# Optimization experiments

Hardware: AMD Instinct MI355X
Metric: run time of the kernel (lower is better)

Reference implementation:

```python
import jax, jax.numpy as jnp
import numpy as np

NUM_T = 1000      # diffusion timesteps
TIME_DIM = 16     # gaussian time embedding size
DIST_DIM = 16     # gaussian distance embedding size


def _gsmear(x, stop, num_g):
    # GaussianSmearing with linearly spaced centers in [0, stop]
    offsets = jnp.linspace(0.0, stop, num_g)
    coeff = -0.5 / (offsets[1] - offsets[0]) ** 2
    return jnp.exp(coeff * (x[:, None] - offsets[None, :]) ** 2)


def setup_inputs():
    key = jax.random.key(0)
    ks = jax.random.split(key, 20)
    N, EH, G = 20000, 100000, 1000          # nodes, halfedges, graphs
    NT, ND, ED, L, NE = 16, 256, 128, 2, 5   # node types, node_dim, edge_dim, blocks, edge types
    h_node = jax.nn.one_hot(jax.random.randint(ks[0], (N,), 0, NT), NT, dtype=jnp.float32)
    pos_node = jax.random.normal(ks[1], (N, 3), dtype=jnp.float32) * 3.0
    batch_node = jnp.sort(jax.random.randint(ks[2], (N,), 0, G))
    half = jax.random.randint(ks[3], (2, EH), 0, N)
    edge_index = jnp.concatenate([half, half[::-1]], axis=1)  # halfedges + flipped
    bh = jnp.sort(jax.random.randint(ks[4], (EH,), 0, G))
    batch_edge = jnp.concatenate([bh, bh], axis=0)
    t = jax.random.randint(ks[5], (G,), 0, NUM_T)

    def w(k, shape):
        fan_in = shape[-2] if len(shape) > 1 else shape[-1]
        return jax.random.normal(k, shape, dtype=jnp.float32) / np.sqrt(fan_in)

    e_in = ED + 2 * ND + DIST_DIM + 1
    return {
        'h_node': h_node, 'pos_node': pos_node, 'batch_node': batch_node,
        'edge_index': edge_index, 'batch_edge': batch_edge, 't': t,
        'W_node_emb': w(ks[6], (NT, ND - TIME_DIM)),
        'W_edge_emb': w(ks[7], (2 * NT, ED - TIME_DIM)),
        'We1': w(ks[8], (L, e_in, ED)), 'be1': jnp.zeros((L, ED), jnp.float32),
        'We2': w(ks[9], (L, ED, ED)), 'be2': jnp.zeros((L, ED), jnp.float32),
        'Wm': w(ks[10], (L, ND + ED, ND)), 'bm': jnp.zeros((L, ND), jnp.float32),
        'Wn1': w(ks[11], (L, 2 * ND + 1, ND)), 'bn1': jnp.zeros((L, ND), jnp.float32),
        'Wn2': w(ks[12], (L, ND, ND)), 'bn2': jnp.zeros((L, ND), jnp.float32),
        'Wd1': w(ks[13], (ED + ND, ED)), 'bd1': jnp.zeros((ED,), jnp.float32),
        'Wd2': w(ks[14], (ED, ED)), 'bd2': jnp.zeros((ED,), jnp.float32),
        'Wd3': w(ks[15], (ED, NE)), 'bd3': jnp.zeros((NE,), jnp.float32),
    }


def reference(h_node, pos_node, batch_node, edge_index, batch_edge, t,
              W_node_emb, W_edge_emb, We1, be1, We2, be2, Wm, bm,
              Wn1, bn1, Wn2, bn2, Wd1, bd1, Wd2, bd2, Wd3, bd3):
    src, dst = edge_index[0], edge_index[1]
    N = h_node.shape[0]
    L = We1.shape[0]

    # edge input features: concat of endpoint node features (gather)
    h_e0 = jnp.concatenate([h_node[src], h_node[dst]], axis=-1)

    tn = t[batch_node].astype(jnp.float32)  # per-node timestep
    te = t[batch_edge].astype(jnp.float32)  # per-edge timestep
    # linear embed + gaussian-smeared time embedding
    h_n = jnp.concatenate([h_node @ W_node_emb, _gsmear(tn, float(NUM_T), TIME_DIM)], axis=-1)
    h_e = jnp.concatenate([h_e0 @ W_edge_emb, _gsmear(te, float(NUM_T), TIME_DIM)], axis=-1)
    node_time = (tn / NUM_T)[:, None]
    edge_time = (te / NUM_T)[:, None]

    # geometric edge features
    d = jnp.linalg.norm(pos_node[dst] - pos_node[src], axis=-1)
    dist_emb = _gsmear(d, 10.0, DIST_DIM)

    # NodeEdgeNet: alternating edge / node residual updates
    for l in range(L):
        e_in = jnp.concatenate([h_e, h_n[src], h_n[dst], dist_emb, edge_time], axis=-1)
        h_e = h_e + jax.nn.relu(e_in @ We1[l] + be1[l]) @ We2[l] + be2[l]
        msg = jax.nn.relu(jnp.concatenate([h_n[src], h_e], axis=-1) @ Wm[l] + bm[l])
        agg = jax.ops.segment_sum(msg, dst, num_segments=N)
        n_in = jnp.concatenate([h_n, agg, node_time], axis=-1)
        h_n = h_n + jax.nn.relu(n_in @ Wn1[l] + bn1[l]) @ Wn2[l] + bn2[l]

    # symmetrize halfedges and decode edge types
    nh = h_e.shape[0] // 2
    h_ext = jnp.concatenate([h_e[:nh] + h_e[nh:],
                             h_n[src[:nh]] + h_n[dst[:nh]]], axis=-1)
    h = jax.nn.relu(h_ext @ Wd1 + bd1)
    h = jax.nn.relu(h @ Wd2 + bd2)
    return h @ Wd3 + bd3
```

## Files before the change

### kernel.cpp

```cpp
#include <hip/hip_runtime.h>
#include <math.h>


typedef __attribute__((ext_vector_type(8)))  short bf16x8;
typedef __attribute__((ext_vector_type(16))) float f32x16;

__device__ __forceinline__ float b2f(unsigned short u) {
    union { float f; unsigned int i; } x; x.i = ((unsigned int)u) << 16; return x.f;
}
__device__ __forceinline__ unsigned short f2b(float f) {
    union { float f; unsigned int i; } x; x.f = f;
    unsigned int r = x.i + 0x7fffu + ((x.i >> 16) & 1u);
    return (unsigned short)(r >> 16);
}
__device__ __forceinline__ bf16x8 ld8(const unsigned short* p) { return *(const bf16x8*)p; }
__device__ __forceinline__ bf16x8 zero8() { bf16x8 r = {0,0,0,0,0,0,0,0}; return r; }
__device__ __forceinline__ bf16x8 add8(bf16x8 a, bf16x8 b) {
    bf16x8 r;
#pragma unroll
    for (int j = 0; j < 8; j++) r[j] = (short)f2b(b2f((unsigned short)a[j]) + b2f((unsigned short)b[j]));
    return r;
}

#define MFMA4(ACC, A0, A1, B0, B1)                                                   \
    ACC[0][0] = __builtin_amdgcn_mfma_f32_32x32x16_bf16(A0, B0, ACC[0][0], 0, 0, 0); \
    ACC[0][1] = __builtin_amdgcn_mfma_f32_32x32x16_bf16(A0, B1, ACC[0][1], 0, 0, 0); \
    ACC[1][0] = __builtin_amdgcn_mfma_f32_32x32x16_bf16(A1, B0, ACC[1][0], 0, 0, 0); \
    ACC[1][1] = __builtin_amdgcn_mfma_f32_32x32x16_bf16(A1, B1, ACC[1][1], 0, 0, 0);

#define LANE_SETUP()                                  \
    const int tid  = threadIdx.x;                     \
    const int lane = tid & 63;                        \
    const int wave = tid >> 6;                        \
    const int wm = wave >> 1, wn = wave & 1;          \
    const int l31 = lane & 31, l5 = lane >> 5;        \
    (void)wm; (void)wn; (void)lane;

#define PIPELINE4(NITER, FETCH, ACC)                                  \
    {                                                                 \
        bf16x8 pa0[2], pb0[2], pa1[2], pb1[2], pa2[2], pb2[2];        \
        FETCH(0, pa0, pb0);                                           \
        if (1 < (NITER)) FETCH(1, pa1, pb1);                          \
        _Pragma("unroll")                                             \
        for (int i = 0; i < (NITER); i++) {                           \
            if (i + 2 < (NITER)) FETCH(i + 2, pa2, pb2);              \
            MFMA4(ACC, pa0[0], pa0[1], pb0[0], pb0[1]);               \
            pa0[0] = pa1[0]; pa0[1] = pa1[1];                         \
            pb0[0] = pb1[0]; pb0[1] = pb1[1];                         \
            pa1[0] = pa2[0]; pa1[1] = pa2[1];                         \
            pb1[0] = pb2[0]; pb1[1] = pb2[1];                         \
        }                                                             \
    }

#define PIPELINE2(NITER, FETCH, ACC)                                  \
    {                                                                 \
        bf16x8 pa0, pb0[2], pa1, pb1[2], pa2, pb2[2];                 \
        FETCH(0, pa0, pb0);                                           \
        if (1 < (NITER)) FETCH(1, pa1, pb1);                          \
        _Pragma("unroll")                                             \
        for (int i = 0; i < (NITER); i++) {                           \
            if (i + 2 < (NITER)) FETCH(i + 2, pa2, pb2);              \
            ACC[0] = __builtin_amdgcn_mfma_f32_32x32x16_bf16(pa0, pb0[0], ACC[0], 0, 0, 0); \
            ACC[1] = __builtin_amdgcn_mfma_f32_32x32x16_bf16(pa0, pb0[1], ACC[1], 0, 0, 0); \
            pa0 = pa1; pb0[0] = pb1[0]; pb0[1] = pb1[1];              \
            pa1 = pa2; pb1[0] = pb2[0]; pb1[1] = pb2[1];              \
        }                                                             \
    }

__global__ void zero_i32_k(int* p, int n) {
    int i = blockIdx.x * 256 + threadIdx.x;
    if (i < n) p[i] = 0;
}
__global__ void hist_k(const int* __restrict__ dst, int* __restrict__ cnt, int E) {
    int e = blockIdx.x * 256 + threadIdx.x;
    if (e < E) atomicAdd(&cnt[dst[e]], 1);
}
__global__ __launch_bounds__(256) void scan_k(int* __restrict__ cnt, int N) {
    __shared__ int s[256];
    const int tidx  = threadIdx.x;
    const int chunk = (N + 255) / 256;
    const int lo = tidx * chunk;
    const int hi = (lo + chunk < N) ? lo + chunk : N;
    int sum = 0;
    for (int i = lo; i < hi; i++) sum += cnt[i];
    s[tidx] = sum;
    __syncthreads();
    for (int d = 1; d < 256; d <<= 1) {
        int t = (tidx >= d) ? s[tidx - d] : 0;
        __syncthreads();
        s[tidx] += t;
        __syncthreads();
    }
    int base = s[tidx] - sum;
    for (int i = lo; i < hi; i++) {
        int c = cnt[i];
        cnt[i] = base;
        base += c;
    }
}
__global__ void fill_k(const int* __restrict__ src, const int* __restrict__ dst,
                       const int* __restrict__ batch_edge, int* __restrict__ cur,
                       int* __restrict__ eids, int* __restrict__ pos,
                       int* __restrict__ srcp, int* __restrict__ dstp,
                       int* __restrict__ bep, int E) {
    int e = blockIdx.x * 256 + threadIdx.x;
    if (e < E) {
        int p = atomicAdd(&cur[dst[e]], 1);
        eids[p] = e;
        pos[e]  = p;
        srcp[p] = src[e];
        dstp[p] = dst[e];
        bep[p]  = batch_edge[e];
    }
}
__global__ void pad_k(int* eids, int* srcp, int* dstp, int* bep, int E, int Epad) {
    int i = E + blockIdx.x * 256 + threadIdx.x;
    if (i < Epad) { eids[i] = -1; srcp[i] = 0; dstp[i] = -1; bep[i] = 0; }
}

__global__ void typ_k(const float* __restrict__ h_node, int* __restrict__ typ, int N) {
    int i = blockIdx.x * 256 + threadIdx.x;
    if (i >= N) return;
    int ty = 0;
#pragma unroll
    for (int k = 0; k < 16; k++) if (h_node[i * 16 + k] > 0.5f) ty = k;
    typ[i] = ty;
}

struct TrDesc { const float* W; unsigned short* Wt; int K, N, Kpad; };
struct TrAll  { TrDesc d[12]; };

__global__ __launch_bounds__(256) void tr_all_k(TrAll a) {
    TrDesc t = a.d[blockIdx.y];
    int total = t.N * t.Kpad;
    for (int i = blockIdx.x * 256 + threadIdx.x; i < total; i += gridDim.x * 256) {
        int n = i / t.Kpad, k = i - n * t.Kpad;
        float v = (k < t.K) ? t.W[(size_t)k * t.N + n] : 0.f;
        t.Wt[(size_t)n * t.Kpad + k] = f2b(v);
    }
}

__global__ void embed_node_k(const int* __restrict__ typ,
                             const float* __restrict__ Wn,
                             const int* __restrict__ batch_node,
                             const int* __restrict__ t,
                             unsigned short* __restrict__ h_n, int N) {
    int idx = blockIdx.x * 256 + threadIdx.x;
    if (idx >= N * 32) return;
    int row = idx >> 5, seg = idx & 31;
    bf16x8 v;
    if (seg < 30) {
        const float* w = Wn + (size_t)typ[row] * 240 + seg * 8;
#pragma unroll
        for (int j = 0; j < 8; j++) v[j] = (short)f2b(w[j]);
    } else {
        float x = (float)t[batch_node[row]];
#pragma unroll
        for (int j = 0; j < 8; j++) {
            int col = seg * 8 + j;
            float dx = x - (1000.0f / 15.0f) * (float)(col - 240);
            v[j] = (short)f2b(expf(-1.125e-4f * dx * dx));
        }
    }
    *(bf16x8*)&h_n[(size_t)row * 256 + seg * 8] = v;
}

__global__ void embed_edge_k(const int* __restrict__ typ,
                             const float* __restrict__ We,
                             const int* __restrict__ srcp,
                             const int* __restrict__ dstp,
                             const int* __restrict__ bep,
                             const int* __restrict__ t,
                             unsigned short* __restrict__ h_e, int E) {
    int idx = blockIdx.x * 256 + threadIdx.x;
    if (idx >= E * 16) return;
    int row = idx >> 4, seg = idx & 15;
    bf16x8 v;
    if (seg < 14) {
        int d0 = dstp[row]; if (d0 < 0) d0 = 0;
        const float* ws = We + (size_t)typ[srcp[row]] * 112 + seg * 8;
        const float* wd = We + (size_t)(16 + typ[d0]) * 112 + seg * 8;
#pragma unroll
        for (int j = 0; j < 8; j++) v[j] = (short)f2b(ws[j] + wd[j]);
    } else {
        float x = (float)t[bep[row]];
#pragma unroll
        for (int j = 0; j < 8; j++) {
            int col = seg * 8 + j;
            float dx = x - (1000.0f / 15.0f) * (float)(col - 112);
            v[j] = (short)f2b(expf(-1.125e-4f * dx * dx));
        }
    }
    *(bf16x8*)&h_e[(size_t)row * 128 + seg * 8] = v;
}

__global__ __launch_bounds__(256) void edge_fused_k(
    unsigned short* __restrict__ h_e, const unsigned short* __restrict__ h_n,
    const unsigned short* __restrict__ Wt1, const float* __restrict__ be1,
    const unsigned short* __restrict__ Wt2, const float* __restrict__ be2,
    const float* __restrict__ pos, const int* __restrict__ srcp,
    const int* __restrict__ dstp, const int* __restrict__ t,
    const int* __restrict__ bep, int E)
{
    __shared__ __align__(16) unsigned short H[128][136];
    LANE_SETUP();
    const int row0 = blockIdx.x * 128;

    int   rr[2]; const unsigned short *hep[2], *hns[2], *hnd[2];
    float dist[2], timev[2]; bool ok[2];
    rr[0] = row0 + wm * 64 + l31; rr[1] = rr[0] + 32;
#pragma unroll
    for (int h = 0; h < 2; h++) {
        ok[h] = rr[h] < E;
        int r = ok[h] ? rr[h] : 0;
        int s = srcp[r], d = dstp[r] < 0 ? 0 : dstp[r];
        hep[h] = h_e + (size_t)r * 128;
        hns[h] = h_n + (size_t)s * 256;
        hnd[h] = h_n + (size_t)d * 256;
        float dx = pos[d * 3 + 0] - pos[s * 3 + 0];
        float dy = pos[d * 3 + 1] - pos[s * 3 + 1];
        float dz = pos[d * 3 + 2] - pos[s * 3 + 2];
        dist[h]  = sqrtf(dx * dx + dy * dy + dz * dz);
        timev[h] = (float)t[bep[r]] * 1e-3f;
    }

    const unsigned short* W1a = Wt1 + (size_t)(wn * 64 + l31) * 672;
    const unsigned short* W1b = Wt1 + (size_t)(wn * 64 + 32 + l31) * 672;

    f32x16 acc[2][2] = {};
#define EF_FETCH(i, A, B)                                                      \
    {                                                                          \
        const int c = 2 * (i) + l5;                                            \
        _Pragma("unroll")                                                      \
        for (int h = 0; h < 2; h++) {                                          \
            if (!ok[h])      A[h] = zero8();                                   \
            else if (c < 16) A[h] = ld8(hep[h] + (c << 3));                    \
            else if (c < 48) A[h] = ld8(hns[h] + ((c - 16) << 3));             \
            else if (c < 80) A[h] = ld8(hnd[h] + ((c - 48) << 3));             \
            else if (c < 82) {                                                 \
                bf16x8 rv;                                                     \
                _Pragma("unroll")                                              \
                for (int j = 0; j < 8; j++) {                                  \
                    float u = dist[h] - (10.0f / 15.0f) * (float)((c - 80) * 8 + j); \
                    rv[j] = (short)f2b(expf(-1.125f * u * u));                 \
                }                                                              \
                A[h] = rv;                                                     \
            } else if (c == 82) { A[h] = zero8(); A[h][0] = (short)f2b(timev[h]); } \
            else A[h] = zero8();                                               \
        }                                                                      \
        B[0] = ld8(W1a + (c << 3));                                            \
        B[1] = ld8(W1b + (c << 3));                                            \
    }
    PIPELINE4(42, EF_FETCH, acc)
#undef EF_FETCH

#pragma unroll
    for (int mt = 0; mt < 2; mt++)
#pragma unroll
        for (int nt = 0; nt < 2; nt++)
#pragma unroll
            for (int r = 0; r < 16; r++) {
                int lrow = wm * 64 + mt * 32 + (r & 3) + 8 * (r >> 2) + 4 * l5;
                int col  = wn * 64 + nt * 32 + l31;
                float v = acc[mt][nt][r] + be1[col];
                H[lrow][col] = f2b(fmaxf(v, 0.f));
            }
    __syncthreads();

    const unsigned short* W2a = Wt2 + (size_t)(wn * 64 + l31) * 128;
    const unsigned short* W2b = Wt2 + (size_t)(wn * 64 + 32 + l31) * 128;
    f32x16 acc2[2][2] = {};
#define EF2_FETCH(i, A, B)                                          \
    {                                                               \
        const int c = 2 * (i) + l5;                                 \
        A[0] = *(const bf16x8*)&H[wm * 64 + l31][c << 3];           \
        A[1] = *(const bf16x8*)&H[wm * 64 + 32 + l31][c << 3];      \
        B[0] = ld8(W2a + (c << 3));                                 \
        B[1] = ld8(W2b + (c << 3));                                 \
    }
    PIPELINE4(8, EF2_FETCH, acc2)
#undef EF2_FETCH

#pragma unroll
    for (int mt = 0; mt < 2; mt++)
#pragma unroll
        for (int nt = 0; nt < 2; nt++)
#pragma unroll
            for (int r = 0; r < 16; r++) {
                int lrow = wm * 64 + mt * 32 + (r & 3) + 8 * (r >> 2) + 4 * l5;
                int grow = row0 + lrow;
                if (grow >= E) continue;
                int col = wn * 64 + nt * 32 + l31;
                size_t off = (size_t)grow * 128 + col;
                float v = acc2[mt][nt][r] + be2[col] + b2f(h_e[off]);
                h_e[off] = f2b(v);
            }
}

__global__ __launch_bounds__(256) void msg_k(
    const unsigned short* __restrict__ h_e, const unsigned short* __restrict__ h_n,
    const unsigned short* __restrict__ Wtm, const float* __restrict__ bm,
    const int* __restrict__ srcp, const int* __restrict__ dstp,
    float* __restrict__ agg, int E, int nRowTiles)
{
    __shared__ __align__(16) char smem[33024 + 512];
    unsigned short (*As)[8][8] = (unsigned short(*)[8][8])smem;
    unsigned short (*Bs)[8][8] = (unsigned short(*)[8][8])(smem + 16384);
    float (*T)[129] = (float(*)[129])smem;
    int* dstv = (int*)(smem + 33024);

    LANE_SETUP();
    const int b    = blockIdx.x;
    const int rowt = (b >> 4) * 8 + (b & 7);
    const int colh = (b >> 3) & 1;
    if (rowt >= nRowTiles) return;
    const int row0 = rowt * 128;
    const int col0 = colh * 128;

    if (tid < 128) dstv[tid] = dstp[row0 + tid];

    const int srow = tid >> 3, sks = tid & 7;

    f32x16 acc[2][2] = {};
    for (int kc = 0; kc < 6; kc++) {
        const int cg = kc * 8 + sks;
#pragma unroll
        for (int p = 0; p < 4; p++) {
            int row = srow + p * 32;
            int r   = row0 + row;
            bf16x8 v;
            if (r < E) {
                if (cg < 32) v = ld8(h_n + (size_t)srcp[r] * 256 + (cg << 3));
                else         v = ld8(h_e + (size_t)r * 128 + ((cg - 32) << 3));
            } else v = zero8();
            *(bf16x8*)&As[row][sks ^ (row & 7)][0] = v;
        }
#pragma unroll
        for (int p = 0; p < 4; p++) {
            int col = srow + p * 32;
            bf16x8 v = ld8(Wtm + (size_t)(col0 + col) * 384 + (cg << 3));
            *(bf16x8*)&Bs[col][sks ^ (col & 7)][0] = v;
        }
        __syncthreads();
#pragma unroll
        for (int s = 0; s < 4; s++) {
            const int ks  = s * 2 + l5;
            const int ra0 = wm * 64 + l31, ra1 = ra0 + 32;
            const int ca0 = wn * 64 + l31, ca1 = ca0 + 32;
            bf16x8 a0 = *(const bf16x8*)&As[ra0][ks ^ (ra0 & 7)][0];
            bf16x8 a1 = *(const bf16x8*)&As[ra1][ks ^ (ra1 & 7)][0];
            bf16x8 b0 = *(const bf16x8*)&Bs[ca0][ks ^ (ca0 & 7)][0];
            bf16x8 b1 = *(const bf16x8*)&Bs[ca1][ks ^ (ca1 & 7)][0];
            MFMA4(acc, a0, a1, b0, b1);
        }
        __syncthreads();
    }

    for (int ph = 0; ph < 2; ph++) {
        __syncthreads();
        if (wm == ph) {
#pragma unroll
            for (int mt = 0; mt < 2; mt++)
#pragma unroll
                for (int nt = 0; nt < 2; nt++)
#pragma unroll
                    for (int r = 0; r < 16; r++) {
                        int lrow = mt * 32 + (r & 3) + 8 * (r >> 2) + 4 * l5;
                        int col  = wn * 64 + nt * 32 + l31;
                        T[lrow][col] = acc[mt][nt][r] + bm[col0 + col];
                    }
        }
        __syncthreads();
        const int col = tid & 127, seg = tid >> 7;
        const int gcol = col0 + col;
        float run = 0.f; int prev = -1;
#pragma unroll 4
        for (int i = 0; i < 32; i++) {
            int lr = seg * 32 + i;
            int d  = dstv[ph * 64 + lr];
            float v = fmaxf(T[lr][col], 0.f);
            if (d != prev) {
                if (prev >= 0 && run != 0.f) atomicAdd(&agg[(size_t)prev * 256 + gcol], run);
                run = 0.f; prev = d;
            }
            if (d >= 0) run += v;
        }
        if (prev >= 0 && run != 0.f) atomicAdd(&agg[(size_t)prev * 256 + gcol], run);
    }
}

__global__ __launch_bounds__(256) void nin_k(
    const unsigned short* __restrict__ h_n, const float* __restrict__ agg,
    const unsigned short* __restrict__ Wtn1, const float* __restrict__ bn1,
    const int* __restrict__ batch_node, const int* __restrict__ t,
    unsigned short* __restrict__ Hn, int N)
{
    LANE_SETUP();
    const int row0 = blockIdx.x * 64;
    const int col0 = blockIdx.y * 128;

    int rr = row0 + wm * 32 + l31;
    bool ok = rr < N;
    int r = ok ? rr : 0;
    float timev = (float)t[batch_node[r]] * 1e-3f;
    const unsigned short* hp = h_n + (size_t)r * 256;
    const float*          ap = agg + (size_t)r * 256;

    const unsigned short* Wa = Wtn1 + (size_t)(col0 + wn * 64 + l31) * 544;
    const unsigned short* Wb = Wtn1 + (size_t)(col0 + wn * 64 + 32 + l31) * 544;

    f32x16 acc[2] = {};
#define NIN_FETCH(i, A, B)                                              \
    {                                                                   \
        const int c = 2 * (i) + l5;                                     \
        if (!ok) A = zero8();                                           \
        else if (c < 32) A = ld8(hp + (c << 3));                        \
        else if (c < 64) {                                              \
            const float* q = ap + ((c - 32) << 3);                      \
            bf16x8 v;                                                   \
            _Pragma("unroll")                                           \
            for (int j = 0; j < 8; j++) v[j] = (short)f2b(q[j]);        \
            A = v;                                                      \
        } else if (c == 64) { A = zero8(); A[0] = (short)f2b(timev); }  \
        else A = zero8();                                               \
        B[0] = ld8(Wa + (c << 3));                                      \
        B[1] = ld8(Wb + (c << 3));                                      \
    }
    PIPELINE2(34, NIN_FETCH, acc)
#undef NIN_FETCH

#pragma unroll
    for (int nt = 0; nt < 2; nt++)
#pragma unroll
        for (int r2 = 0; r2 < 16; r2++) {
            int lrow = wm * 32 + (r2 & 3) + 8 * (r2 >> 2) + 4 * l5;
            int grow = row0 + lrow;
            if (grow >= N) continue;
            int col = col0 + wn * 64 + nt * 32 + l31;
            float v = fmaxf(acc[nt][r2] + bn1[col], 0.f);
            Hn[(size_t)grow * 256 + col] = f2b(v);
        }
}

__global__ __launch_bounds__(256) void node_plain_k(
    const unsigned short* __restrict__ Hn, const unsigned short* __restrict__ Wtn2,
    const float* __restrict__ bn2, unsigned short* __restrict__ h_n, int N)
{
    LANE_SETUP();
    const int row0 = blockIdx.x * 64;
    const int col0 = blockIdx.y * 128;

    int rr = row0 + wm * 32 + l31;
    bool ok = rr < N;
    const unsigned short* hp = Hn + (size_t)(ok ? rr : 0) * 256;

    const unsigned short* Wa = Wtn2 + (size_t)(col0 + wn * 64 + l31) * 256;
    const unsigned short* Wb = Wtn2 + (size_t)(col0 + wn * 64 + 32 + l31) * 256;

    f32x16 acc[2] = {};
#define NP_FETCH(i, A, B)                          \
    {                                              \
        const int c = 2 * (i) + l5;                \
        A = ok ? ld8(hp + (c << 3)) : zero8();     \
        B[0] = ld8(Wa + (c << 3));                 \
        B[1] = ld8(Wb + (c << 3));                 \
    }
    PIPELINE2(16, NP_FETCH, acc)
#undef NP_FETCH

#pragma unroll
    for (int nt = 0; nt < 2; nt++)
#pragma unroll
        for (int r2 = 0; r2 < 16; r2++) {
            int lrow = wm * 32 + (r2 & 3) + 8 * (r2 >> 2) + 4 * l5;
            int grow = row0 + lrow;
            if (grow >= N) continue;
            int col = col0 + wn * 64 + nt * 32 + l31;
            size_t off = (size_t)grow * 256 + col;
            float v = acc[nt][r2] + bn2[col] + b2f(h_n[off]);
            h_n[off] = f2b(v);
        }
}

__global__ __launch_bounds__(256) void dec_fused_k(
    const unsigned short* __restrict__ h_e, const unsigned short* __restrict__ h_n,
    const unsigned short* __restrict__ Wtd1, const float* __restrict__ bd1,
    const unsigned short* __restrict__ Wtd2, const float* __restrict__ bd2,
    const float* __restrict__ Wd3, const float* __restrict__ bd3,
    const int* __restrict__ src, const int* __restrict__ dst,
    const int* __restrict__ pos, float* __restrict__ out, int nh)
{
    __shared__ __align__(16) unsigned short H1[128][136];
    __shared__ __align__(16) unsigned short H2[128][136];
    LANE_SETUP();
    const int row0 = blockIdx.x * 128;

    int rr[2]; const unsigned short *he1[2], *he2[2], *hns[2], *hnd[2]; bool ok[2];
    rr[0] = row0 + wm * 64 + l31; rr[1] = rr[0] + 32;
#pragma unroll
    for (int h = 0; h < 2; h++) {
        ok[h] = rr[h] < nh;
        int r = ok[h] ? rr[h] : 0;
        he1[h] = h_e + (size_t)pos[r] * 128;
        he2[h] = h_e + (size_t)pos[r + nh] * 128;
        hns[h] = h_n + (size_t)src[r] * 256;
        hnd[h] = h_n + (size_t)dst[r] * 256;
    }

    const unsigned short* W1a = Wtd1 + (size_t)(wn * 64 + l31) * 384;
    const unsigned short* W1b = Wtd1 + (size_t)(wn * 64 + 32 + l31) * 384;

    f32x16 acc[2][2] = {};
#define DC_FETCH(i, A, B)                                                            \
    {                                                                                \
        const int c = 2 * (i) + l5;                                                  \
        _Pragma("unroll")                                                            \
        for (int h = 0; h < 2; h++) {                                                \
            if (!ok[h])      A[h] = zero8();                                         \
            else if (c < 16) A[h] = add8(ld8(he1[h] + (c << 3)), ld8(he2[h] + (c << 3))); \
            else             A[h] = add8(ld8(hns[h] + ((c - 16) << 3)), ld8(hnd[h] + ((c - 16) << 3))); \
        }                                                                            \
        B[0] = ld8(W1a + (c << 3));                                                  \
        B[1] = ld8(W1b + (c << 3));                                                  \
    }
    PIPELINE4(24, DC_FETCH, acc)
#undef DC_FETCH

#pragma unroll
    for (int mt = 0; mt < 2; mt++)
#pragma unroll
        for (int nt = 0; nt < 2; nt++)
#pragma unroll
            for (int r = 0; r < 16; r++) {
                int lrow = wm * 64 + mt * 32 + (r & 3) + 8 * (r >> 2) + 4 * l5;
                int col  = wn * 64 + nt * 32 + l31;
                H1[lrow][col] = f2b(fmaxf(acc[mt][nt][r] + bd1[col], 0.f));
            }
    __syncthreads();

    const unsigned short* W2a = Wtd2 + (size_t)(wn * 64 + l31) * 128;
    const unsigned short* W2b = Wtd2 + (size_t)(wn * 64 + 32 + l31) * 128;
    f32x16 acc2[2][2] = {};
#define DC2_FETCH(i, A, B)                                          \
    {                                                               \
        const int c = 2 * (i) + l5;                                 \
        A[0] = *(const bf16x8*)&H1[wm * 64 + l31][c << 3];          \
        A[1] = *(const bf16x8*)&H1[wm * 64 + 32 + l31][c << 3];     \
        B[0] = ld8(W2a + (c << 3));                                 \
        B[1] = ld8(W2b + (c << 3));                                 \
    }
    PIPELINE4(8, DC2_FETCH, acc2)
#undef DC2_FETCH

#pragma unroll
    for (int mt = 0; mt < 2; mt++)
#pragma unroll
        for (int nt = 0; nt < 2; nt++)
#pragma unroll
            for (int r = 0; r < 16; r++) {
                int lrow = wm * 64 + mt * 32 + (r & 3) + 8 * (r >> 2) + 4 * l5;
                int col  = wn * 64 + nt * 32 + l31;
                H2[lrow][col] = f2b(fmaxf(acc2[mt][nt][r] + bd2[col], 0.f));
            }
    __syncthreads();

    if (tid < 128) {
        int grow = row0 + tid;
        if (grow < nh) {
            float a5[5] = {0.f, 0.f, 0.f, 0.f, 0.f};
            for (int ks = 0; ks < 16; ks++) {
                bf16x8 hv = *(const bf16x8*)&H2[tid][ks << 3];
#pragma unroll
                for (int j = 0; j < 8; j++) {
                    float a = b2f((unsigned short)hv[j]);
                    int   k = ks * 8 + j;
#pragma unroll
                    for (int c5 = 0; c5 < 5; c5++) a5[c5] += a * Wd3[k * 5 + c5];
                }
            }
#pragma unroll
            for (int c5 = 0; c5 < 5; c5++) out[(size_t)grow * 5 + c5] = a5[c5] + bd3[c5];
        }
    }
}


__global__ void zero_k(float* p, long n) {
    long i = (long)blockIdx.x * 256 + threadIdx.x;
    if (i < n) p[i] = 0.f;
}


extern "C" void kernel_launch(void* const* d_in, const int* in_sizes, int n_in,
                              void* d_out, int out_size, void* d_ws, size_t ws_size,
                              hipStream_t stream) {
    const float* h_node     = (const float*)d_in[0];
    const float* pos_node   = (const float*)d_in[1];
    const int*   batch_node = (const int*)d_in[2];
    const int*   edge_index = (const int*)d_in[3];
    const int*   batch_edge = (const int*)d_in[4];
    const int*   t          = (const int*)d_in[5];
    const float* W_node_emb = (const float*)d_in[6];
    const float* W_edge_emb = (const float*)d_in[7];
    const float* We1 = (const float*)d_in[8];
    const float* be1 = (const float*)d_in[9];
    const float* We2 = (const float*)d_in[10];
    const float* be2 = (const float*)d_in[11];
    const float* Wm  = (const float*)d_in[12];
    const float* bm  = (const float*)d_in[13];
    const float* Wn1 = (const float*)d_in[14];
    const float* bn1 = (const float*)d_in[15];
    const float* Wn2 = (const float*)d_in[16];
    const float* bn2 = (const float*)d_in[17];
    const float* Wd1 = (const float*)d_in[18];
    const float* bd1 = (const float*)d_in[19];
    const float* Wd2 = (const float*)d_in[20];
    const float* bd2 = (const float*)d_in[21];
    const float* Wd3 = (const float*)d_in[22];
    const float* bd3 = (const float*)d_in[23];

    const int N  = in_sizes[0] / 16;
    const int E  = in_sizes[3] / 2;
    const int nh = E / 2;
    const int* src = edge_index;
    const int* dst = edge_index + E;

    const int gE   = (E + 127) / 128;
    const int gE8  = ((gE + 7) / 8) * 8;
    const int gN64 = (N + 63) / 64;
    const int Epad = gE * 128;

    float* agg  = (float*)d_ws;
    int*   cnt  = (int*)(agg + (size_t)N * 256);
    int*   eids = cnt + N;
    int*   pos  = eids + Epad;
    int*   srcp = pos + Epad;
    int*   dstp = srcp + Epad;
    int*   bep  = dstp + Epad;
    int*   typ  = bep + Epad;
    unsigned short* h_e = (unsigned short*)(typ + N);
    unsigned short* h_n = h_e + (size_t)E * 128;
    unsigned short* Hn  = h_n + (size_t)N * 256;
    unsigned short* Wt1  = Hn + (size_t)N * 256;
    unsigned short* Wt2  = Wt1 + 2 * 128 * 672;
    unsigned short* Wtm  = Wt2 + 2 * 128 * 128;
    unsigned short* Wtn1 = Wtm + 2 * 256 * 384;
    unsigned short* Wtn2 = Wtn1 + 2 * 256 * 544;
    unsigned short* Wtd1 = Wtn2 + 2 * 256 * 256;
    unsigned short* Wtd2 = Wtd1 + 128 * 384;

    zero_i32_k<<<(N + 255) / 256, 256, 0, stream>>>(cnt, N);
    hist_k<<<(E + 255) / 256, 256, 0, stream>>>(dst, cnt, E);
    scan_k<<<1, 256, 0, stream>>>(cnt, N);
    fill_k<<<(E + 255) / 256, 256, 0, stream>>>(src, dst, batch_edge, cnt,
                                                eids, pos, srcp, dstp, bep, E);
    if (Epad > E) pad_k<<<1, 256, 0, stream>>>(eids, srcp, dstp, bep, E, Epad);
    typ_k<<<(N + 255) / 256, 256, 0, stream>>>(h_node, typ, N);

    TrAll ta;
    for (int l = 0; l < 2; l++) {
        ta.d[l * 5 + 0] = { We1 + (size_t)l * 657 * 128, Wt1 + (size_t)l * 128 * 672, 657, 128, 672 };
        ta.d[l * 5 + 1] = { We2 + (size_t)l * 128 * 128, Wt2 + (size_t)l * 128 * 128, 128, 128, 128 };
        ta.d[l * 5 + 2] = { Wm  + (size_t)l * 384 * 256, Wtm + (size_t)l * 256 * 384, 384, 256, 384 };
        ta.d[l * 5 + 3] = { Wn1 + (size_t)l * 513 * 256, Wtn1 + (size_t)l * 256 * 544, 513, 256, 544 };
        ta.d[l * 5 + 4] = { Wn2 + (size_t)l * 256 * 256, Wtn2 + (size_t)l * 256 * 256, 256, 256, 256 };
    }
    ta.d[10] = { Wd1, Wtd1, 384, 128, 384 };
    ta.d[11] = { Wd2, Wtd2, 128, 128, 128 };
    tr_all_k<<<dim3(48, 12), 256, 0, stream>>>(ta);

    embed_node_k<<<(N * 32 + 255) / 256, 256, 0, stream>>>(typ, W_node_emb, batch_node, t, h_n, N);
    embed_edge_k<<<(E * 16 + 255) / 256, 256, 0, stream>>>(typ, W_edge_emb, srcp, dstp, bep, t, h_e, E);

    for (int l = 0; l < 2; l++) {
        edge_fused_k<<<gE, 256, 0, stream>>>(
            h_e, h_n, Wt1 + (size_t)l * 128 * 672, be1 + l * 128,
            Wt2 + (size_t)l * 128 * 128, be2 + l * 128,
            pos_node, srcp, dstp, t, bep, E);

        zero_k<<<(int)(((long)N * 256 + 255) / 256), 256, 0, stream>>>(agg, (long)N * 256);
        msg_k<<<gE8 * 2, 256, 0, stream>>>(
            h_e, h_n, Wtm + (size_t)l * 256 * 384, bm + l * 256, srcp, dstp, agg, E, gE);

        nin_k<<<dim3(gN64, 2), 256, 0, stream>>>(
            h_n, agg, Wtn1 + (size_t)l * 256 * 544, bn1 + l * 256, batch_node, t, Hn, N);

        node_plain_k<<<dim3(gN64, 2), 256, 0, stream>>>(
            Hn, Wtn2 + (size_t)l * 256 * 256, bn2 + l * 256, h_n, N);
    }

    dec_fused_k<<<(nh + 127) / 128, 256, 0, stream>>>(
        h_e, h_n, Wtd1, bd1, Wtd2, bd2, Wd3, bd3, src, dst, pos, (float*)d_out, nh);
}
```

Measured before the change: 1.027 ms.

## Stage gathered edge and decoder inputs through swizzled shared memory tiles

The first GEMM of the edge and decoder kernels now stages both the gathered A rows and the weight B tiles into XOR-swizzled shared memory in K-chunks of 64, rather than each wave loading A and B fragments straight from global memory. Each row and weight element is fetched once per block instead of once per wave that uses it, which removes the duplicate gather traffic across the wave grid. In exchange the kernels add two barriers per K-chunk and lose the register-prefetch pipeline, so load latency is no longer overlapped with MFMA work. The distance embedding is now recomputed per chunk inside the loader.

```diff
diff --git a/kernel.cpp b/kernel.cpp
--- a/kernel.cpp
+++ b/kernel.cpp
@@ -202,57 +202,76 @@
     const int* __restrict__ dstp, const int* __restrict__ t,
     const int* __restrict__ bep, int E)
 {
-    __shared__ __align__(16) unsigned short H[128][136];
+    __shared__ __align__(16) char smem[128 * 136 * 2];
+    unsigned short (*As)[8][8] = (unsigned short(*)[8][8])smem;
+    unsigned short (*Bs)[8][8] = (unsigned short(*)[8][8])(smem + 16384);
+    unsigned short (*H)[136]   = (unsigned short(*)[136])smem;
+
     LANE_SETUP();
     const int row0 = blockIdx.x * 128;
-
-    int   rr[2]; const unsigned short *hep[2], *hns[2], *hnd[2];
-    float dist[2], timev[2]; bool ok[2];
-    rr[0] = row0 + wm * 64 + l31; rr[1] = rr[0] + 32;
-#pragma unroll
-    for (int h = 0; h < 2; h++) {
-        ok[h] = rr[h] < E;
-        int r = ok[h] ? rr[h] : 0;
-        int s = srcp[r], d = dstp[r] < 0 ? 0 : dstp[r];
-        hep[h] = h_e + (size_t)r * 128;
-        hns[h] = h_n + (size_t)s * 256;
-        hnd[h] = h_n + (size_t)d * 256;
-        float dx = pos[d * 3 + 0] - pos[s * 3 + 0];
-        float dy = pos[d * 3 + 1] - pos[s * 3 + 1];
-        float dz = pos[d * 3 + 2] - pos[s * 3 + 2];
-        dist[h]  = sqrtf(dx * dx + dy * dy + dz * dz);
-        timev[h] = (float)t[bep[r]] * 1e-3f;
-    }
-
-    const unsigned short* W1a = Wt1 + (size_t)(wn * 64 + l31) * 672;
-    const unsigned short* W1b = Wt1 + (size_t)(wn * 64 + 32 + l31) * 672;
+    const int srow = tid >> 3, sks = tid & 7;
+
+    int rge[4], sg[4], dg[4]; bool okr[4];
+#pragma unroll
+    for (int p = 0; p < 4; p++) {
+        int r = row0 + srow + p * 32;
+        okr[p] = r < E;
+        rge[p] = okr[p] ? r : 0;
+        sg[p]  = srcp[rge[p]];
+        dg[p]  = dstp[rge[p]]; if (dg[p] < 0) dg[p] = 0;
+    }
 
     f32x16 acc[2][2] = {};
-#define EF_FETCH(i, A, B)                                                      \
-    {                                                                          \
-        const int c = 2 * (i) + l5;                                            \
-        _Pragma("unroll")                                                      \
-        for (int h = 0; h < 2; h++) {                                          \
-            if (!ok[h])      A[h] = zero8();                                   \
-            else if (c < 16) A[h] = ld8(hep[h] + (c << 3));                    \
-            else if (c < 48) A[h] = ld8(hns[h] + ((c - 16) << 3));             \
-            else if (c < 80) A[h] = ld8(hnd[h] + ((c - 48) << 3));             \
-            else if (c < 82) {                                                 \
-                bf16x8 rv;                                                     \
-                _Pragma("unroll")                                              \
-                for (int j = 0; j < 8; j++) {                                  \
-                    float u = dist[h] - (10.0f / 15.0f) * (float)((c - 80) * 8 + j); \
-                    rv[j] = (short)f2b(expf(-1.125f * u * u));                 \
-                }                                                              \
-                A[h] = rv;                                                     \
-            } else if (c == 82) { A[h] = zero8(); A[h][0] = (short)f2b(timev[h]); } \
-            else A[h] = zero8();                                               \
-        }                                                                      \
-        B[0] = ld8(W1a + (c << 3));                                            \
-        B[1] = ld8(W1b + (c << 3));                                            \
-    }
-    PIPELINE4(42, EF_FETCH, acc)
-#undef EF_FETCH
+    for (int kc = 0; kc < 11; kc++) {
+        const int cg = kc * 8 + sks;
+#pragma unroll
+        for (int p = 0; p < 4; p++) {
+            int row = srow + p * 32;
+            bf16x8 v;
+            if (!okr[p] || cg >= 83) {
+                v = zero8();
+            } else if (cg < 16) {
+                v = ld8(h_e + (size_t)rge[p] * 128 + (cg << 3));
+            } else if (cg < 48) {
+                v = ld8(h_n + (size_t)sg[p] * 256 + ((cg - 16) << 3));
+            } else if (cg < 80) {
+                v = ld8(h_n + (size_t)dg[p] * 256 + ((cg - 48) << 3));
+            } else if (cg < 82) {
+                float dx = pos[dg[p] * 3 + 0] - pos[sg[p] * 3 + 0];
+                float dy = pos[dg[p] * 3 + 1] - pos[sg[p] * 3 + 1];
+                float dz = pos[dg[p] * 3 + 2] - pos[sg[p] * 3 + 2];
+                float dist = sqrtf(dx * dx + dy * dy + dz * dz);
+#pragma unroll
+                for (int j = 0; j < 8; j++) {
+                    float u = dist - (10.0f / 15.0f) * (float)((cg - 80) * 8 + j);
+                    v[j] = (short)f2b(expf(-1.125f * u * u));
+                }
+            } else {
+                v = zero8();
+                v[0] = (short)f2b((float)t[bep[rge[p]]] * 1e-3f);
+            }
+            *(bf16x8*)&As[row][sks ^ (row & 7)][0] = v;
+        }
+#pragma unroll
+        for (int p = 0; p < 4; p++) {
+            int col = srow + p * 32;
+            bf16x8 v = (cg < 84) ? ld8(Wt1 + (size_t)col * 672 + (cg << 3)) : zero8();
+            *(bf16x8*)&Bs[col][sks ^ (col & 7)][0] = v;
+        }
+        __syncthreads();
+#pragma unroll
+        for (int s = 0; s < 4; s++) {
+            const int ks  = s * 2 + l5;
+            const int ra0 = wm * 64 + l31, ra1 = ra0 + 32;
+            const int ca0 = wn * 64 + l31, ca1 = ca0 + 32;
+            bf16x8 a0 = *(const bf16x8*)&As[ra0][ks ^ (ra0 & 7)][0];
+            bf16x8 a1 = *(const bf16x8*)&As[ra1][ks ^ (ra1 & 7)][0];
+            bf16x8 b0 = *(const bf16x8*)&Bs[ca0][ks ^ (ca0 & 7)][0];
+            bf16x8 b1 = *(const bf16x8*)&Bs[ca1][ks ^ (ca1 & 7)][0];
+            MFMA4(acc, a0, a1, b0, b1);
+        }
+        __syncthreads();
+    }
 
 #pragma unroll
     for (int mt = 0; mt < 2; mt++)
@@ -490,41 +509,60 @@
     const int* __restrict__ src, const int* __restrict__ dst,
     const int* __restrict__ pos, float* __restrict__ out, int nh)
 {
-    __shared__ __align__(16) unsigned short H1[128][136];
+    __shared__ __align__(16) char smem[128 * 136 * 2];
     __shared__ __align__(16) unsigned short H2[128][136];
+    unsigned short (*As)[8][8] = (unsigned short(*)[8][8])smem;
+    unsigned short (*Bs)[8][8] = (unsigned short(*)[8][8])(smem + 16384);
+    unsigned short (*H1)[136]  = (unsigned short(*)[136])smem;
+
     LANE_SETUP();
     const int row0 = blockIdx.x * 128;
-
-    int rr[2]; const unsigned short *he1[2], *he2[2], *hns[2], *hnd[2]; bool ok[2];
-    rr[0] = row0 + wm * 64 + l31; rr[1] = rr[0] + 32;
-#pragma unroll
-    for (int h = 0; h < 2; h++) {
-        ok[h] = rr[h] < nh;
-        int r = ok[h] ? rr[h] : 0;
-        he1[h] = h_e + (size_t)pos[r] * 128;
-        he2[h] = h_e + (size_t)pos[r + nh] * 128;
-        hns[h] = h_n + (size_t)src[r] * 256;
-        hnd[h] = h_n + (size_t)dst[r] * 256;
-    }
-
-    const unsigned short* W1a = Wtd1 + (size_t)(wn * 64 + l31) * 384;
-    const unsigned short* W1b = Wtd1 + (size_t)(wn * 64 + 32 + l31) * 384;
+    const int srow = tid >> 3, sks = tid & 7;
+
+    const unsigned short *pe1[4], *pe2[4], *pns[4], *pnd[4]; bool okr[4];
+#pragma unroll
+    for (int p = 0; p < 4; p++) {
+        int r = row0 + srow + p * 32;
+        okr[p] = r < nh;
+        int rg = okr[p] ? r : 0;
+        pe1[p] = h_e + (size_t)pos[rg] * 128;
+        pe2[p] = h_e + (size_t)pos[rg + nh] * 128;
+        pns[p] = h_n + (size_t)src[rg] * 256;
+        pnd[p] = h_n + (size_t)dst[rg] * 256;
+    }
 
     f32x16 acc[2][2] = {};
-#define DC_FETCH(i, A, B)                                                            \
-    {                                                                                \
-        const int c = 2 * (i) + l5;                                                  \
-        _Pragma("unroll")                                                            \
-        for (int h = 0; h < 2; h++) {                                                \
-            if (!ok[h])      A[h] = zero8();                                         \
-            else if (c < 16) A[h] = add8(ld8(he1[h] + (c << 3)), ld8(he2[h] + (c << 3))); \
-            else             A[h] = add8(ld8(hns[h] + ((c - 16) << 3)), ld8(hnd[h] + ((c - 16) << 3))); \
-        }                                                                            \
-        B[0] = ld8(W1a + (c << 3));                                                  \
-        B[1] = ld8(W1b + (c << 3));                                                  \
-    }
-    PIPELINE4(24, DC_FETCH, acc)
-#undef DC_FETCH
+    for (int kc = 0; kc < 6; kc++) {
+        const int cg = kc * 8 + sks;
+#pragma unroll
+        for (int p = 0; p < 4; p++) {
+            int row = srow + p * 32;
+            bf16x8 v;
+            if (!okr[p]) v = zero8();
+            else if (cg < 16) v = add8(ld8(pe1[p] + (cg << 3)), ld8(pe2[p] + (cg << 3)));
+            else              v = add8(ld8(pns[p] + ((cg - 16) << 3)), ld8(pnd[p] + ((cg - 16) << 3)));
+            *(bf16x8*)&As[row][sks ^ (row & 7)][0] = v;
+        }
+#pragma unroll
+        for (int p = 0; p < 4; p++) {
+            int col = srow + p * 32;
+            bf16x8 v = ld8(Wtd1 + (size_t)col * 384 + (cg << 3));
+            *(bf16x8*)&Bs[col][sks ^ (col & 7)][0] = v;
+        }
+        __syncthreads();
+#pragma unroll
+        for (int s = 0; s < 4; s++) {
+            const int ks  = s * 2 + l5;
+            const int ra0 = wm * 64 + l31, ra1 = ra0 + 32;
+            const int ca0 = wn * 64 + l31, ca1 = ca0 + 32;
+            bf16x8 a0 = *(const bf16x8*)&As[ra0][ks ^ (ra0 & 7)][0];
+            bf16x8 a1 = *(const bf16x8*)&As[ra1][ks ^ (ra1 & 7)][0];
+            bf16x8 b0 = *(const bf16x8*)&Bs[ca0][ks ^ (ca0 & 7)][0];
+            bf16x8 b1 = *(const bf16x8*)&Bs[ca1][ks ^ (ca1 & 7)][0];
+            MFMA4(acc, a0, a1, b0, b1);
+        }
+        __syncthreads();
+    }
 
 #pragma unroll
     for (int mt = 0; mt < 2; mt++)
```

Measured after the change: 962.0 us. -6.3%, faster.
